# Kernel tuning notes

Measured on AMD Instinct MI355X. Metric: run time of the kernel, lower is better.

Reference implementation:

```python
import jax, jax.numpy as jnp
import numpy as np

B, S, H, NH, DK, VOCAB, FF, L = 512, 64, 512, 8, 64, 2000, 2048, 6


def _pos_enc():
    pos = jnp.arange(S, dtype=jnp.float32)[:, None]           # [S,1]
    i = jnp.arange(H // 2, dtype=jnp.float32)                  # [H/2]
    ang = pos / (10000.0 ** (2.0 * i / H))                     # [S,H/2]
    pe = jnp.zeros((S, H), jnp.float32)
    pe = pe.at[:, 0::2].set(jnp.sin(ang)).at[:, 1::2].set(jnp.cos(ang))
    return pe


def _ln(x, g, b, eps=1e-5):
    m = x.mean(-1, keepdims=True)
    v = ((x - m) ** 2).mean(-1, keepdims=True)
    return (x - m) / jnp.sqrt(v + eps) * g + b


def _heads(x, w):  # x:[B,S,H] w:[H,H] -> [B,NH,S,DK]
    return (x @ w.T).reshape(B, S, NH, DK).transpose(0, 2, 1, 3)


def _sdpa(Q, K, V, keep):  # keep: bool mask broadcastable to [B,NH,S,S]
    scores = jnp.einsum('bhqd,bhkd->bhqk', Q, K) / np.sqrt(DK).astype(np.float32)
    scores = jnp.where(keep, scores, -1e9)
    return jnp.einsum('bhqk,bhkd->bhqd', jax.nn.softmax(scores, axis=-1), V)


def _merge(z, wo):  # [B,NH,S,DK] -> [B,S,H] -> out proj
    return z.transpose(0, 2, 1, 3).reshape(B, S, H) @ wo.T


def setup_inputs():
    key = jax.random.key(0)
    ks = jax.random.split(key, 30)
    n = lambda k, sh: jax.random.normal(k, sh, jnp.float32) * 0.02
    inp = {
        'source_ids': jax.random.randint(ks[0], (B, S), 0, VOCAB),
        'target_ids': jax.random.randint(ks[1], (B, S), 0, VOCAB),
        'source_mask': jnp.ones((B, S), jnp.int32),
        'target_mask': jnp.ones((B, S), jnp.int32),
        'src_emb': n(ks[2], (VOCAB, H)),
        'tgt_emb': n(ks[3], (VOCAB, H)),
        'enc_wq': n(ks[4], (L, H, H)), 'enc_wk': n(ks[5], (L, H, H)),
        'enc_wv': n(ks[6], (L, H, H)), 'enc_wo': n(ks[7], (L, H, H)),
        'enc_ln_g': jnp.ones((L, H), jnp.float32), 'enc_ln_b': jnp.zeros((L, H), jnp.float32),
        'enc_fc1_w': n(ks[8], (L, FF, H)), 'enc_fc1_b': jnp.zeros((L, FF), jnp.float32),
        'enc_fc2_w': n(ks[9], (L, H, FF)), 'enc_fc2_b': jnp.zeros((L, H), jnp.float32),
        'dec_mwq': n(ks[10], (L, H, H)), 'dec_mwk': n(ks[11], (L, H, H)),
        'dec_mwv': n(ks[12], (L, H, H)), 'dec_mwo': n(ks[13], (L, H, H)),
        'dec_cwq': n(ks[14], (L, H, H)), 'dec_cwo': n(ks[15], (L, H, H)),
        'dec_ln_g': jnp.ones((L, H), jnp.float32), 'dec_ln_b': jnp.zeros((L, H), jnp.float32),
        'dec_fc_w': n(ks[16], (L, H, H)), 'dec_fc_b': jnp.zeros((L, H), jnp.float32),
    }
    return inp


def reference(source_ids, target_ids, source_mask, target_mask, src_emb, tgt_emb,
              enc_wq, enc_wk, enc_wv, enc_wo, enc_ln_g, enc_ln_b,
              enc_fc1_w, enc_fc1_b, enc_fc2_w, enc_fc2_b,
              dec_mwq, dec_mwk, dec_mwv, dec_mwo, dec_cwq, dec_cwo,
              dec_ln_g, dec_ln_b, dec_fc_w, dec_fc_b):
    pe = _pos_enc()
    x = src_emb[source_ids] + pe              # [B,S,H]
    y = tgt_emb[target_ids] + pe
    src_keep = (source_mask != 0)[:, None, None, :]                 # [B,1,1,S]
    causal = jnp.tril(jnp.ones((S, S), bool))
    tgt_keep = (target_mask != 0)[:, None, None, :] & causal[None, None]  # [B,1,S,S]

    Kenc = Venc = None
    for l in range(L):
        Q, K, Vh = _heads(x, enc_wq[l]), _heads(x, enc_wk[l]), _heads(x, enc_wv[l])
        z = _merge(_sdpa(Q, K, Vh, src_keep), enc_wo[l])
        x = _ln(x + z, enc_ln_g[l], enc_ln_b[l])
        f = (x @ enc_fc1_w[l].T + enc_fc1_b[l]) @ enc_fc2_w[l].T + enc_fc2_b[l]
        x = _ln(x + f, enc_ln_g[l], enc_ln_b[l])
        Kenc, Venc = K, Vh  # last encoder block's K,V feed decoder cross-attn

    for l in range(L):
        Q, K, Vh = _heads(y, dec_mwq[l]), _heads(y, dec_mwk[l]), _heads(y, dec_mwv[l])
        z1 = _merge(_sdpa(Q, K, Vh, tgt_keep), dec_mwo[l])
        t1 = _ln(y + z1, dec_ln_g[l], dec_ln_b[l])
        Qc = _heads(t1, dec_cwq[l])
        # NOTE: original applies the TARGET mask to encoder keys (faithful)
        z2 = _merge(_sdpa(Qc, Kenc, Venc, tgt_keep), dec_cwo[l])
        t2 = _ln(t1 + z2, dec_ln_g[l], dec_ln_b[l])
        t3 = t2 @ dec_fc_w[l].T + dec_fc_b[l]
        y = _ln(t2 + t3, dec_ln_g[l], dec_ln_b[l])
    return y
```

## Files before the change

### kernel.cpp

```cpp
#include <hip/hip_runtime.h>

typedef unsigned short u16;
typedef u16 u16x8 __attribute__((ext_vector_type(8)));
typedef __bf16 bf16x8 __attribute__((ext_vector_type(8)));
typedef float f32x4 __attribute__((ext_vector_type(4)));

#define TTOK 32768
#define HD 512
#define FFD 2048
#define SLEN 64
#define EW 262144

__device__ __forceinline__ float b2f(u16 u) {
  union { float f; unsigned int i; } v; v.i = ((unsigned int)u) << 16; return v.f;
}
__device__ __forceinline__ u16 f2b(float f) {
  union { float f; unsigned int i; } v; v.f = f;
  unsigned int i = v.i;
  return (u16)((i + 0x7FFFu + ((i >> 16) & 1u)) >> 16);
}

__device__ __forceinline__ void gload16(const u16* g, u16* l) {
  __builtin_amdgcn_global_load_lds((const __attribute__((address_space(1))) void*)g,
                                   (__attribute__((address_space(3))) void*)l,
                                   16, 0, 0);
}

__device__ __forceinline__ f32x4 mfma16(bf16x8 a, bf16x8 b, f32x4 c) {
  return __builtin_amdgcn_mfma_f32_16x16x32_bf16(a, b, c, 0, 0, 0);
}

__global__ __launch_bounds__(256) void pe_kernel(float* __restrict__ pe) {
  int idx = blockIdx.x * 256 + threadIdx.x;
  int s = idx >> 9, h = idx & 511;
  float e2i = (float)(h & ~1);
  float ang = (float)s * powf(10000.0f, -e2i * (1.0f / 512.0f));
  pe[idx] = (h & 1) ? cosf(ang) : sinf(ang);
}

__global__ __launch_bounds__(256) void wconv_kernel(
    const float* __restrict__ src, u16* __restrict__ dst,
    unsigned int npl, unsigned int dstride) {
  size_t i = ((size_t)blockIdx.x * 256 + threadIdx.x) * 8;
  unsigned int l = (unsigned int)(i / npl);
  unsigned int r = (unsigned int)(i - (size_t)l * npl);
  f32x4 a = *(const f32x4*)(src + i), b = *(const f32x4*)(src + i + 4);
  u16x8 o;
  #pragma unroll
  for (int k = 0; k < 4; ++k) { o[k] = f2b(a[k]); o[4 + k] = f2b(b[k]); }
  *(u16x8*)(dst + (size_t)l * dstride + r) = o;
}

__global__ __launch_bounds__(256) void embed_kernel(
    const int* __restrict__ ids, const float* __restrict__ emb,
    const float* __restrict__ pe, u16* __restrict__ outB) {
  int chunk = blockIdx.x * 256 + threadIdx.x;
  int t = chunk >> 6;
  int c8 = (chunk & 63) * 8;
  int s = t & (SLEN - 1);
  int id = ids[t];
  const float* e = emb + (size_t)id * HD + c8;
  const float* p = pe + s * HD + c8;
  f32x4 e0 = *(const f32x4*)e, e1 = *(const f32x4*)(e + 4);
  f32x4 p0 = *(const f32x4*)p, p1 = *(const f32x4*)(p + 4);
  u16x8 ob;
  #pragma unroll
  for (int i = 0; i < 4; ++i) {
    ob[i]     = f2b(e0[i] + p0[i]);
    ob[4 + i] = f2b(e1[i] + p1[i]);
  }
  *(u16x8*)(outB + (size_t)t * HD + c8) = ob;
}

__global__ __launch_bounds__(256) void kvsave_kernel(
    const u16* __restrict__ src, u16* __restrict__ dst) {
  int idx = blockIdx.x * 256 + threadIdx.x;
  int t = idx >> 7, c = (idx & 127) * 8;
  *(u16x8*)(dst + (size_t)t * 1024 + c) =
      *(const u16x8*)(src + (size_t)t * 1536 + 512 + c);
}

template<int F32OUT>
__global__ __launch_bounds__(256) void ln_kernel(
    const u16* A, const u16* __restrict__ Z, int ldz,
    const float* __restrict__ g, const float* __restrict__ b,
    u16* outB, float* outF) {
  int row = blockIdx.x * 4 + (threadIdx.x >> 6);
  int lane = threadIdx.x & 63;
  size_t base = (size_t)row * HD + lane * 8;
  size_t zbase = (size_t)row * ldz + lane * 8;
  u16x8 av = *(const u16x8*)(A + base);
  u16x8 zv = *(const u16x8*)(Z + zbase);
  float x[8];
  float s = 0.f;
  #pragma unroll
  for (int i = 0; i < 8; ++i) { x[i] = b2f(av[i]) + b2f(zv[i]); s += x[i]; }
  #pragma unroll
  for (int off = 32; off; off >>= 1) s += __shfl_xor(s, off);
  float m = s * (1.0f / HD);
  float vs = 0.f;
  #pragma unroll
  for (int i = 0; i < 8; ++i) { float d = x[i] - m; vs += d * d; }
  #pragma unroll
  for (int off = 32; off; off >>= 1) vs += __shfl_xor(vs, off);
  float rstd = rsqrtf(vs * (1.0f / HD) + 1e-5f);
  f32x4 g0 = *(const f32x4*)(g + lane * 8), g1 = *(const f32x4*)(g + lane * 8 + 4);
  f32x4 b0 = *(const f32x4*)(b + lane * 8), b1 = *(const f32x4*)(b + lane * 8 + 4);
  float o[8];
  #pragma unroll
  for (int i = 0; i < 4; ++i) {
    o[i]     = (x[i] - m) * rstd * g0[i] + b0[i];
    o[4 + i] = (x[4 + i] - m) * rstd * g1[i] + b1[i];
  }
  if (F32OUT) {
    f32x4 o0, o1;
    #pragma unroll
    for (int i = 0; i < 4; ++i) { o0[i] = o[i]; o1[i] = o[4 + i]; }
    *(f32x4*)(outF + base) = o0;
    *(f32x4*)(outF + base + 4) = o1;
  } else {
    u16x8 ob;
    #pragma unroll
    for (int i = 0; i < 8; ++i) ob[i] = f2b(o[i]);
    *(u16x8*)(outB + base) = ob;
  }
}

#define BAR() __builtin_amdgcn_s_barrier()
#define WAIT_LGKM0() asm volatile("s_waitcnt lgkmcnt(0)" ::: "memory")
#define WAIT_VM8()   asm volatile("s_waitcnt vmcnt(8)" ::: "memory")

template<int BIAS, int ACC>
__global__ __launch_bounds__(512, 2) void gemm256(
    const u16* __restrict__ A, const u16* __restrict__ Bw,
    const float* __restrict__ bias, u16* __restrict__ Cb,
    int nbn, int K, int lda, int ldb, int ldc) {
  __shared__ u16 lds[65536];
  const int tid = threadIdx.x;
  const int lane = tid & 63, w = tid >> 6;
  const int wr = w >> 2, wc = w & 3;
  const int l15 = lane & 15, lq = lane >> 4;

  const int cpx = gridDim.x >> 3;
  const int L = (blockIdx.x & 7) * cpx + (blockIdx.x >> 3);
  const int bm = (L / nbn) * 256, bn = (L % nbn) * 256;

  const u16 *pa0, *pa1, *pb0, *pb1;
  {
    int p0 = w * 1024 + lane * 16;
    int p1 = p0 + 8192;
    int lb0 = p0 ^ (((p0 >> 7) & 7) << 4);
    int lb1 = p1 ^ (((p1 >> 7) & 7) << 4);
    int r0 = (lb0 >> 7) + (((lb0 >> 6) & 1) << 7);
    int r1 = (lb1 >> 7) + (((lb1 >> 6) & 1) << 7);
    int c0 = (lb0 & 63) >> 1;
    int c1 = (lb1 & 63) >> 1;
    pa0 = A  + (size_t)(bm + r0) * lda + c0;
    pa1 = A  + (size_t)(bm + r1) * lda + c1;
    pb0 = Bw + (size_t)(bn + r0) * ldb + c0;
    pb1 = Bw + (size_t)(bn + r1) * ldb + c1;
  }
  const int dst = w * 512;

  int offA[8], offB[4];
  #pragma unroll
  for (int mf = 0; mf < 8; ++mf) {
    int rowp = mf * 16 + l15;
    offA[mf] = ((rowp * 128 + wr * 64 + lq * 16) ^ ((l15 & 7) << 4)) >> 1;
  }
  #pragma unroll
  for (int j = 0; j < 4; ++j) {
    int rB = wc * 64 + j * 16 + l15;
    int rowp = rB & 127, cg = rB >> 7;
    offB[j] = ((rowp * 128 + cg * 64 + lq * 16) ^ ((l15 & 7) << 4)) >> 1;
  }

  const int NK2 = K >> 5;
  const int NT  = K >> 6;

#define STAGEA(kh, slot) { \
    gload16(pa0 + (kh) * 32, &lds[(slot) * 8192 + dst]); \
    gload16(pa1 + (kh) * 32, &lds[(slot) * 8192 + dst + 4096]); }
#define STAGEB(kh, slot) { \
    gload16(pb0 + (kh) * 32, &lds[32768 + (slot) * 8192 + dst]); \
    gload16(pb1 + (kh) * 32, &lds[32768 + (slot) * 8192 + dst + 4096]); }
#define LDA4(slot, mh) { \
    _Pragma("unroll") for (int i = 0; i < 4; ++i) \
      af[i] = *(const bf16x8*)&lds[(slot) * 8192 + offA[(mh) * 4 + i]]; }
#define LDB4(slot) { \
    _Pragma("unroll") for (int j = 0; j < 4; ++j) \
      bf[j] = *(const bf16x8*)&lds[32768 + (slot) * 8192 + offB[j]]; }
#define MFMA16(mh) { \
    __builtin_amdgcn_s_setprio(1); \
    _Pragma("unroll") for (int i = 0; i < 4; ++i) \
      _Pragma("unroll") for (int j = 0; j < 4; ++j) \
        acc[(mh) * 4 + i][j] = mfma16(af[i], bf[j], acc[(mh) * 4 + i][j]); \
    __builtin_amdgcn_s_setprio(0); }

  f32x4 acc[8][4] = {};
  bf16x8 af[4], bf[4];

  STAGEA(0, 0); STAGEB(0, 0);
  STAGEA(1, 1); STAGEB(1, 1);
  STAGEA(2, 2); STAGEB(2, 2);
  WAIT_VM8();
  BAR();

  for (int t = 0; t < NT; ++t) {
    const int s0 = (2 * t) & 3, s1 = (2 * t + 1) & 3;
    int kh3 = 2 * t + 3; if (kh3 > NK2 - 1) kh3 = NK2 - 1;
    int kh4 = 2 * t + 4; if (kh4 > NK2 - 1) kh4 = NK2 - 1;
    const int w3 = (2 * t + 3) & 3, w4 = (2 * t + 4) & 3;

    LDB4(s0); LDA4(s0, 0);
    STAGEA(kh3, w3);
    BAR(); WAIT_LGKM0();
    MFMA16(0);
    BAR();
    LDA4(s0, 1);
    STAGEB(kh3, w3);
    BAR(); WAIT_LGKM0();
    MFMA16(1);
    WAIT_VM8();
    BAR();
    LDB4(s1); LDA4(s1, 0);
    STAGEA(kh4, w4);
    BAR(); WAIT_LGKM0();
    MFMA16(0);
    BAR();
    LDA4(s1, 1);
    STAGEB(kh4, w4);
    BAR(); WAIT_LGKM0();
    MFMA16(1);
    WAIT_VM8();
    BAR();
  }
  asm volatile("s_waitcnt vmcnt(0)" ::: "memory");

  #pragma unroll
  for (int h = 0; h < 2; ++h) {
    BAR();
    if (wr == h) {
      #pragma unroll
      for (int mf = 0; mf < 8; ++mf)
        #pragma unroll
        for (int j = 0; j < 4; ++j)
          #pragma unroll
          for (int r = 0; r < 4; ++r) {
            int row = mf * 16 + lq * 4 + r;
            int col = wc * 64 + j * 16 + l15;
            int byt = (row * 1024 + col * 4) ^ (((row >> 2) & 1) << 6);
            *(float*)((char*)lds + byt) = acc[mf][j][r];
          }
    }
    WAIT_LGKM0();
    BAR();
    #pragma unroll
    for (int k = 0; k < 8; ++k) {
      int c = tid + k * 512;
      int row = c >> 5, c32 = c & 31;
      int byt = (row * 1024 + c32 * 32) ^ (((row >> 2) & 1) << 6);
      f32x4 v0 = *(const f32x4*)((const char*)lds + byt);
      f32x4 v1 = *(const f32x4*)((const char*)lds + byt + 16);
      int gcol = bn + c32 * 8;
      size_t off = (size_t)(bm + h * 128 + row) * ldc + gcol;
      if (BIAS) {
        f32x4 bb0 = *(const f32x4*)(bias + gcol);
        f32x4 bb1 = *(const f32x4*)(bias + gcol + 4);
        #pragma unroll
        for (int i = 0; i < 4; ++i) { v0[i] += bb0[i]; v1[i] += bb1[i]; }
      }
      u16x8 ob;
      if (ACC) {
        u16x8 cr = *(const u16x8*)(Cb + off);
        #pragma unroll
        for (int i = 0; i < 4; ++i) {
          ob[i]     = f2b(v0[i] + b2f(cr[i]));
          ob[4 + i] = f2b(v1[i] + b2f(cr[4 + i]));
        }
      } else {
        #pragma unroll
        for (int i = 0; i < 4; ++i) { ob[i] = f2b(v0[i]); ob[4 + i] = f2b(v1[i]); }
      }
      *(u16x8*)(Cb + off) = ob;
    }
  }
#undef STAGEA
#undef STAGEB
#undef LDA4
#undef LDB4
#undef MFMA16
}

template<int CAUSAL>
__global__ __launch_bounds__(256) void attn_kernel(
    u16* Q, const u16* __restrict__ Kb, const u16* __restrict__ Vb,
    const int* __restrict__ mask, int qld, int kvld) {
  __shared__ u16 Ks[64 * 72];
  __shared__ u16 Vt[64 * 72];
  __shared__ u16 Ps[4][16 * 72];
  const int bh = blockIdx.x;
  const int b = bh >> 3, h = bh & 7;
  const int h0 = h * 64;
  const int tid = threadIdx.x, lane = tid & 63, w = tid >> 6;
  const size_t qbase = (size_t)b * 64 * qld + h0;
  const size_t kbase = (size_t)b * 64 * kvld + h0;
  const int l15 = lane & 15, l16 = (lane >> 4) * 8;

  {
    int r = tid >> 2;
    int c = (tid & 3) * 16;
    const u16* ksrc = Kb + kbase + (size_t)r * kvld + c;
    *(u16x8*)&Ks[r * 72 + c]     = *(const u16x8*)ksrc;
    *(u16x8*)&Ks[r * 72 + c + 8] = *(const u16x8*)(ksrc + 8);
    const u16* vsrc = Vb + kbase + (size_t)r * kvld + c;
    u16x8 t0 = *(const u16x8*)vsrc;
    u16x8 t1 = *(const u16x8*)(vsrc + 8);
    #pragma unroll
    for (int i = 0; i < 8; ++i) {
      Vt[(c + i) * 72 + r]     = t0[i];
      Vt[(c + 8 + i) * 72 + r] = t1[i];
    }
  }
  const int qrow = w * 16 + l15;
  const u16* qp = Q + qbase + (size_t)qrow * qld;
  bf16x8 qf0 = *(const bf16x8*)&qp[l16];
  bf16x8 qf1 = *(const bf16x8*)&qp[32 + l16];
  __syncthreads();

  f32x4 sc[4] = {};
  #pragma unroll
  for (int nf = 0; nf < 4; ++nf) {
    bf16x8 k0 = *(const bf16x8*)&Ks[(nf * 16 + l15) * 72 + l16];
    bf16x8 k1 = *(const bf16x8*)&Ks[(nf * 16 + l15) * 72 + 32 + l16];
    sc[nf] = mfma16(qf0, k0, sc[nf]);
    sc[nf] = mfma16(qf1, k1, sc[nf]);
  }
  int mk[4];
  #pragma unroll
  for (int nf = 0; nf < 4; ++nf) mk[nf] = mask[b * 64 + nf * 16 + l15];
  float pv[4][4];
  #pragma unroll
  for (int r = 0; r < 4; ++r) {
    int q = w * 16 + (lane >> 4) * 4 + r;
    #pragma unroll
    for (int nf = 0; nf < 4; ++nf) {
      int k = nf * 16 + l15;
      bool kp = (mk[nf] != 0);
      if (CAUSAL) kp = kp && (k <= q);
      pv[r][nf] = kp ? sc[nf][r] * 0.125f : -1e9f;
    }
  }
  #pragma unroll
  for (int r = 0; r < 4; ++r) {
    float mx = fmaxf(fmaxf(pv[r][0], pv[r][1]), fmaxf(pv[r][2], pv[r][3]));
    #pragma unroll
    for (int off = 1; off < 16; off <<= 1) mx = fmaxf(mx, __shfl_xor(mx, off));
    float sum = 0.f;
    #pragma unroll
    for (int nf = 0; nf < 4; ++nf) { pv[r][nf] = __expf(pv[r][nf] - mx); sum += pv[r][nf]; }
    #pragma unroll
    for (int off = 1; off < 16; off <<= 1) sum += __shfl_xor(sum, off);
    float inv = 1.0f / sum;
    #pragma unroll
    for (int nf = 0; nf < 4; ++nf) pv[r][nf] *= inv;
  }
  #pragma unroll
  for (int r = 0; r < 4; ++r) {
    int q = (lane >> 4) * 4 + r;
    #pragma unroll
    for (int nf = 0; nf < 4; ++nf)
      Ps[w][q * 72 + nf * 16 + l15] = f2b(pv[r][nf]);
  }
  f32x4 oacc[4] = {};
  #pragma unroll
  for (int kk = 0; kk < 2; ++kk) {
    bf16x8 pa = *(const bf16x8*)&Ps[w][l15 * 72 + kk * 32 + l16];
    #pragma unroll
    for (int df = 0; df < 4; ++df) {
      bf16x8 vf = *(const bf16x8*)&Vt[(df * 16 + l15) * 72 + kk * 32 + l16];
      oacc[df] = mfma16(pa, vf, oacc[df]);
    }
  }
  #pragma unroll
  for (int df = 0; df < 4; ++df) {
    int col = df * 16 + l15;
    #pragma unroll
    for (int r = 0; r < 4; ++r) {
      int t = w * 16 + (lane >> 4) * 4 + r;
      Q[qbase + (size_t)t * qld + col] = f2b(oacc[df][r]);
    }
  }
}

extern "C" void kernel_launch(void* const* d_in, const int* in_sizes, int n_in,
                              void* d_out, int out_size, void* d_ws, size_t ws_size,
                              hipStream_t stream) {
  const int* src_ids    = (const int*)d_in[0];
  const int* tgt_ids    = (const int*)d_in[1];
  const int* src_mask   = (const int*)d_in[2];
  const int* tgt_mask   = (const int*)d_in[3];
  const float* src_emb  = (const float*)d_in[4];
  const float* tgt_emb  = (const float*)d_in[5];
  const float* enc_wq = (const float*)d_in[6];
  const float* enc_wk = (const float*)d_in[7];
  const float* enc_wv = (const float*)d_in[8];
  const float* enc_wo = (const float*)d_in[9];
  const float* enc_g  = (const float*)d_in[10];
  const float* enc_b  = (const float*)d_in[11];
  const float* fc1w = (const float*)d_in[12];
  const float* fc1b = (const float*)d_in[13];
  const float* fc2w = (const float*)d_in[14];
  const float* fc2b = (const float*)d_in[15];
  const float* mwq = (const float*)d_in[16];
  const float* mwk = (const float*)d_in[17];
  const float* mwv = (const float*)d_in[18];
  const float* mwo = (const float*)d_in[19];
  const float* cwq = (const float*)d_in[20];
  const float* cwo = (const float*)d_in[21];
  const float* dec_g = (const float*)d_in[22];
  const float* dec_b = (const float*)d_in[23];
  const float* dfw = (const float*)d_in[24];
  const float* dfb = (const float*)d_in[25];
  float* outF = (float*)d_out;
  u16* kvenc = (u16*)d_out;

  constexpr size_t SZ_PE  = (size_t)SLEN * HD * 4;
  constexpr size_t SZ_W   = (size_t)114 * EW * 2;
  constexpr size_t SZ_CUR = (size_t)TTOK * HD * 2;
  constexpr size_t SZ_QKV = (size_t)TTOK * 1536 * 2;
  constexpr size_t NEED   = SZ_PE + SZ_W + SZ_CUR + SZ_QKV;
  if (ws_size < NEED) return;

  char* ws = (char*)d_ws;
  float* pe = (float*)ws;
  u16* W    = (u16*)(ws + SZ_PE);
  u16* cur  = (u16*)(ws + SZ_PE + SZ_W);
  u16* qkv  = (u16*)(ws + SZ_PE + SZ_W + SZ_CUR);
  u16* z2   = qkv + (size_t)TTOK * 1024;

  dim3 blk(256), blk5(512);
  const unsigned int E = EW, S_E = 12 * EW, S_D = 7 * EW;
  u16* WD = W + (size_t)72 * EW;

  pe_kernel<<<128, blk, 0, stream>>>(pe);

  wconv_kernel<<<768,  blk, 0, stream>>>(enc_wq, W,          E,     S_E);
  wconv_kernel<<<768,  blk, 0, stream>>>(enc_wk, W + E,      E,     S_E);
  wconv_kernel<<<768,  blk, 0, stream>>>(enc_wv, W + 2 * E,  E,     S_E);
  wconv_kernel<<<768,  blk, 0, stream>>>(enc_wo, W + 3 * E,  E,     S_E);
  wconv_kernel<<<3072, blk, 0, stream>>>(fc1w,   W + 4 * E,  4 * E, S_E);
  wconv_kernel<<<3072, blk, 0, stream>>>(fc2w,   W + 8 * E,  4 * E, S_E);
  wconv_kernel<<<768,  blk, 0, stream>>>(mwq,    WD,         E,     S_D);
  wconv_kernel<<<768,  blk, 0, stream>>>(mwk,    WD + E,     E,     S_D);
  wconv_kernel<<<768,  blk, 0, stream>>>(mwv,    WD + 2 * E, E,     S_D);
  wconv_kernel<<<768,  blk, 0, stream>>>(mwo,    WD + 3 * E, E,     S_D);
  wconv_kernel<<<768,  blk, 0, stream>>>(cwq,    WD + 4 * E, E,     S_D);
  wconv_kernel<<<768,  blk, 0, stream>>>(cwo,    WD + 5 * E, E,     S_D);
  wconv_kernel<<<768,  blk, 0, stream>>>(dfw,    WD + 6 * E, E,     S_D);

  embed_kernel<<<8192, blk, 0, stream>>>(src_ids, src_emb, pe, cur);
  for (int l = 0; l < 6; ++l) {
    const u16* Wl = W + (size_t)l * S_E;
    const float* g  = enc_g + (size_t)l * HD;
    const float* bb = enc_b + (size_t)l * HD;
    const float* b1 = fc1b + (size_t)l * FFD;
    const float* b2 = fc2b + (size_t)l * HD;

    gemm256<0,0><<<768, blk5, 0, stream>>>(cur, Wl, nullptr, qkv, 6, 512, 512, 512, 1536);
    attn_kernel<0><<<4096, blk, 0, stream>>>(qkv, qkv + 512, qkv + 1024, src_mask, 1536, 1536);
    if (l == 5)
      kvsave_kernel<<<16384, blk, 0, stream>>>(qkv, kvenc);
    gemm256<0,0><<<256, blk5, 0, stream>>>(qkv, Wl + 3 * E, nullptr, qkv + 1024, 2, 512, 1536, 512, 1536);
    ln_kernel<0><<<8192, blk, 0, stream>>>(cur, qkv + 1024, 1536, g, bb, cur, nullptr);
    gemm256<1,0><<<512, blk5, 0, stream>>>(cur, Wl + 4 * E, b1,        qkv, 4, 512, 512, 512, 1024);
    gemm256<1,0><<<256, blk5, 0, stream>>>(qkv, Wl + 8 * E, b2,        z2,  2, 1024, 1024, 2048, 512);
    gemm256<1,0><<<512, blk5, 0, stream>>>(cur, Wl + 6 * E, b1 + 1024, qkv, 4, 512, 512, 512, 1024);
    gemm256<0,1><<<256, blk5, 0, stream>>>(qkv, Wl + 8 * E + 1024, nullptr, z2, 2, 1024, 1024, 2048, 512);
    ln_kernel<0><<<8192, blk, 0, stream>>>(cur, z2, 512, g, bb, cur, nullptr);
  }

  embed_kernel<<<8192, blk, 0, stream>>>(tgt_ids, tgt_emb, pe, cur);
  for (int l = 0; l < 6; ++l) {
    const u16* Wl = WD + (size_t)l * S_D;
    const float* g  = dec_g + (size_t)l * HD;
    const float* bb = dec_b + (size_t)l * HD;
    const float* fb = dfb + (size_t)l * HD;

    gemm256<0,0><<<768, blk5, 0, stream>>>(cur, Wl, nullptr, qkv, 6, 512, 512, 512, 1536);
    attn_kernel<1><<<4096, blk, 0, stream>>>(qkv, qkv + 512, qkv + 1024, tgt_mask, 1536, 1536);
    gemm256<0,0><<<256, blk5, 0, stream>>>(qkv, Wl + 3 * E, nullptr, qkv + 1024, 2, 512, 1536, 512, 1536);
    ln_kernel<0><<<8192, blk, 0, stream>>>(cur, qkv + 1024, 1536, g, bb, cur, nullptr);

    gemm256<0,0><<<256, blk5, 0, stream>>>(cur, Wl + 4 * E, nullptr, qkv, 2, 512, 512, 512, 1536);
    attn_kernel<1><<<4096, blk, 0, stream>>>(qkv, kvenc, kvenc + 512, tgt_mask, 1536, 1024);
    gemm256<0,0><<<256, blk5, 0, stream>>>(qkv, Wl + 5 * E, nullptr, qkv + 1024, 2, 512, 1536, 512, 1536);
    ln_kernel<0><<<8192, blk, 0, stream>>>(cur, qkv + 1024, 1536, g, bb, cur, nullptr);

    gemm256<1,0><<<256, blk5, 0, stream>>>(cur, Wl + 6 * E, fb, qkv, 2, 512, 512, 512, 512);
    if (l == 5)
      ln_kernel<1><<<8192, blk, 0, stream>>>(cur, qkv, 512, g, bb, nullptr, outF);
    else
      ln_kernel<0><<<8192, blk, 0, stream>>>(cur, qkv, 512, g, bb, cur, nullptr);
  }
  (void)in_sizes; (void)n_in; (void)out_size;
}
```

Baseline: 3.579 ms.

## Fuse encoder KV save into attention and run full-width FFN when workspace allows

Measured after the change: 3.528 ms. No clear change (-1.4%).

```diff
diff --git a/kernel.cpp b/kernel.cpp
--- a/kernel.cpp
+++ b/kernel.cpp
@@ -70,14 +70,6 @@
     ob[4 + i] = f2b(e1[i] + p1[i]);
   }
   *(u16x8*)(outB + (size_t)t * HD + c8) = ob;
-}
-
-__global__ __launch_bounds__(256) void kvsave_kernel(
-    const u16* __restrict__ src, u16* __restrict__ dst) {
-  int idx = blockIdx.x * 256 + threadIdx.x;
-  int t = idx >> 7, c = (idx & 127) * 8;
-  *(u16x8*)(dst + (size_t)t * 1024 + c) =
-      *(const u16x8*)(src + (size_t)t * 1536 + 512 + c);
 }
 
 template<int F32OUT>
@@ -217,17 +209,20 @@
     BAR(); WAIT_LGKM0();
     MFMA16(0);
     BAR();
+
     LDA4(s0, 1);
     STAGEB(kh3, w3);
     BAR(); WAIT_LGKM0();
     MFMA16(1);
     WAIT_VM8();
     BAR();
+
     LDB4(s1); LDA4(s1, 0);
     STAGEA(kh4, w4);
     BAR(); WAIT_LGKM0();
     MFMA16(0);
     BAR();
+
     LDA4(s1, 1);
     STAGEB(kh4, w4);
     BAR(); WAIT_LGKM0();
@@ -292,10 +287,10 @@
 #undef MFMA16
 }
 
-template<int CAUSAL>
+template<int CAUSAL, int SAVEKV>
 __global__ __launch_bounds__(256) void attn_kernel(
     u16* Q, const u16* __restrict__ Kb, const u16* __restrict__ Vb,
-    const int* __restrict__ mask, int qld, int kvld) {
+    const int* __restrict__ mask, int qld, int kvld, u16* __restrict__ kvdst) {
   __shared__ u16 Ks[64 * 72];
   __shared__ u16 Vt[64 * 72];
   __shared__ u16 Ps[4][16 * 72];
@@ -311,8 +306,10 @@
     int r = tid >> 2;
     int c = (tid & 3) * 16;
     const u16* ksrc = Kb + kbase + (size_t)r * kvld + c;
-    *(u16x8*)&Ks[r * 72 + c]     = *(const u16x8*)ksrc;
-    *(u16x8*)&Ks[r * 72 + c + 8] = *(const u16x8*)(ksrc + 8);
+    u16x8 k0 = *(const u16x8*)ksrc;
+    u16x8 k1 = *(const u16x8*)(ksrc + 8);
+    *(u16x8*)&Ks[r * 72 + c]     = k0;
+    *(u16x8*)&Ks[r * 72 + c + 8] = k1;
     const u16* vsrc = Vb + kbase + (size_t)r * kvld + c;
     u16x8 t0 = *(const u16x8*)vsrc;
     u16x8 t1 = *(const u16x8*)(vsrc + 8);
@@ -320,6 +317,13 @@
     for (int i = 0; i < 8; ++i) {
       Vt[(c + i) * 72 + r]     = t0[i];
       Vt[(c + 8 + i) * 72 + r] = t1[i];
+    }
+    if (SAVEKV) {
+      size_t db = (size_t)(b * 64 + r) * 1024 + h0 + c;
+      *(u16x8*)(kvdst + db)       = k0;
+      *(u16x8*)(kvdst + db + 8)   = k1;
+      *(u16x8*)(kvdst + db + 512) = t0;
+      *(u16x8*)(kvdst + db + 520) = t1;
     }
   }
   const int qrow = w * 16 + l15;
@@ -429,15 +433,20 @@
   constexpr size_t SZ_W   = (size_t)114 * EW * 2;
   constexpr size_t SZ_CUR = (size_t)TTOK * HD * 2;
   constexpr size_t SZ_QKV = (size_t)TTOK * 1536 * 2;
-  constexpr size_t NEED   = SZ_PE + SZ_W + SZ_CUR + SZ_QKV;
-  if (ws_size < NEED) return;
+  constexpr size_t SZ_R   = (size_t)TTOK * FFD * 2;
+  constexpr size_t SZ_Z2  = (size_t)TTOK * HD * 2;
+  constexpr size_t NEED_SMALL = SZ_PE + SZ_W + SZ_CUR + SZ_QKV;
+  constexpr size_t NEED_BIG   = SZ_PE + SZ_W + SZ_CUR + SZ_R + SZ_Z2;
+  if (ws_size < NEED_SMALL) return;
+  const bool big = (ws_size >= NEED_BIG);
 
   char* ws = (char*)d_ws;
   float* pe = (float*)ws;
   u16* W    = (u16*)(ws + SZ_PE);
   u16* cur  = (u16*)(ws + SZ_PE + SZ_W);
   u16* qkv  = (u16*)(ws + SZ_PE + SZ_W + SZ_CUR);
-  u16* z2   = qkv + (size_t)TTOK * 1024;
+  u16* z2   = big ? (u16*)(ws + SZ_PE + SZ_W + SZ_CUR + SZ_R)
+                  : qkv + (size_t)TTOK * 1024;
 
   dim3 blk(256), blk5(512);
   const unsigned int E = EW, S_E = 12 * EW, S_D = 7 * EW;
@@ -468,15 +477,21 @@
     const float* b2 = fc2b + (size_t)l * HD;
 
     gemm256<0,0><<<768, blk5, 0, stream>>>(cur, Wl, nullptr, qkv, 6, 512, 512, 512, 1536);
-    attn_kernel<0><<<4096, blk, 0, stream>>>(qkv, qkv + 512, qkv + 1024, src_mask, 1536, 1536);
     if (l == 5)
-      kvsave_kernel<<<16384, blk, 0, stream>>>(qkv, kvenc);
+      attn_kernel<0,1><<<4096, blk, 0, stream>>>(qkv, qkv + 512, qkv + 1024, src_mask, 1536, 1536, kvenc);
+    else
+      attn_kernel<0,0><<<4096, blk, 0, stream>>>(qkv, qkv + 512, qkv + 1024, src_mask, 1536, 1536, nullptr);
     gemm256<0,0><<<256, blk5, 0, stream>>>(qkv, Wl + 3 * E, nullptr, qkv + 1024, 2, 512, 1536, 512, 1536);
     ln_kernel<0><<<8192, blk, 0, stream>>>(cur, qkv + 1024, 1536, g, bb, cur, nullptr);
-    gemm256<1,0><<<512, blk5, 0, stream>>>(cur, Wl + 4 * E, b1,        qkv, 4, 512, 512, 512, 1024);
-    gemm256<1,0><<<256, blk5, 0, stream>>>(qkv, Wl + 8 * E, b2,        z2,  2, 1024, 1024, 2048, 512);
-    gemm256<1,0><<<512, blk5, 0, stream>>>(cur, Wl + 6 * E, b1 + 1024, qkv, 4, 512, 512, 512, 1024);
-    gemm256<0,1><<<256, blk5, 0, stream>>>(qkv, Wl + 8 * E + 1024, nullptr, z2, 2, 1024, 1024, 2048, 512);
+    if (big) {
+      gemm256<1,0><<<1024, blk5, 0, stream>>>(cur, Wl + 4 * E, b1, qkv, 8, 512, 512, 512, 2048);
+      gemm256<1,0><<<256,  blk5, 0, stream>>>(qkv, Wl + 8 * E, b2, z2, 2, 2048, 2048, 2048, 512);
+    } else {
+      gemm256<1,0><<<512, blk5, 0, stream>>>(cur, Wl + 4 * E, b1,        qkv, 4, 512, 512, 512, 1024);
+      gemm256<1,0><<<256, blk5, 0, stream>>>(qkv, Wl + 8 * E, b2,        z2,  2, 1024, 1024, 2048, 512);
+      gemm256<1,0><<<512, blk5, 0, stream>>>(cur, Wl + 6 * E, b1 + 1024, qkv, 4, 512, 512, 512, 1024);
+      gemm256<0,1><<<256, blk5, 0, stream>>>(qkv, Wl + 8 * E + 1024, nullptr, z2, 2, 1024, 1024, 2048, 512);
+    }
     ln_kernel<0><<<8192, blk, 0, stream>>>(cur, z2, 512, g, bb, cur, nullptr);
   }
 
@@ -488,12 +503,12 @@
     const float* fb = dfb + (size_t)l * HD;
 
     gemm256<0,0><<<768, blk5, 0, stream>>>(cur, Wl, nullptr, qkv, 6, 512, 512, 512, 1536);
-    attn_kernel<1><<<4096, blk, 0, stream>>>(qkv, qkv + 512, qkv + 1024, tgt_mask, 1536, 1536);
+    attn_kernel<1,0><<<4096, blk, 0, stream>>>(qkv, qkv + 512, qkv + 1024, tgt_mask, 1536, 1536, nullptr);
     gemm256<0,0><<<256, blk5, 0, stream>>>(qkv, Wl + 3 * E, nullptr, qkv + 1024, 2, 512, 1536, 512, 1536);
     ln_kernel<0><<<8192, blk, 0, stream>>>(cur, qkv + 1024, 1536, g, bb, cur, nullptr);
 
     gemm256<0,0><<<256, blk5, 0, stream>>>(cur, Wl + 4 * E, nullptr, qkv, 2, 512, 512, 512, 1536);
-    attn_kernel<1><<<4096, blk, 0, stream>>>(qkv, kvenc, kvenc + 512, tgt_mask, 1536, 1024);
+    attn_kernel<1,0><<<4096, blk, 0, stream>>>(qkv, kvenc, kvenc + 512, tgt_mask, 1536, 1024, nullptr);
     gemm256<0,0><<<256, blk5, 0, stream>>>(qkv, Wl + 5 * E, nullptr, qkv + 1024, 2, 512, 1536, 512, 1536);
     ln_kernel<0><<<8192, blk, 0, stream>>>(cur, qkv + 1024, 1536, g, bb, cur, nullptr);
 
```
